# Performance work log

Measured on AMD Instinct MI355X. Metric: run time of the kernel, lower is better.

## Reference

```python
import jax, jax.numpy as jnp
import numpy as np

FRAME = 1024
HOP = 512
BATCH = 64
SAMPLES = 1 << 20


def _make_windows():
    # periodic Hann window; COLA with hop=FRAME//2, normalization constant = 1.0
    n = jnp.arange(FRAME, dtype=jnp.float32)
    w = 0.5 * (1.0 - jnp.cos(2.0 * jnp.pi * n / FRAME))
    # edge_correction loop: only h_idx=1 is non-empty for hop = frame/2
    pre = w.at[: FRAME - HOP].add(w[HOP:])
    post = w.at[HOP:].add(w[: FRAME - HOP])
    # normalize_window with normalization = 1.0 is a no-op; mode='wola' -> sqrt
    return jnp.sqrt(w), jnp.sqrt(pre), jnp.sqrt(post)


def setup_inputs() -> dict:
    key = jax.random.key(0)
    x = jax.random.normal(key, (BATCH, SAMPLES), dtype=jnp.float32)
    w, pre, post = _make_windows()
    return {
        "x": x,
        "window": w,
        "prewindow": pre,
        "postwindow": post,
        "hop_size": HOP,
        "frame_size": FRAME,
    }


def reference(x, window, prewindow, postwindow, hop_size, frame_size):
    # number_of_segments = samples//hop - frame//hop + 1 (as in _segment)
    n_samples = x.shape[1]
    n_seg = n_samples // hop_size - frame_size // hop_size + 1
    # strided gather: idx[k, j] = k*hop + j  -> frames [B, S, F]
    idx = jnp.arange(n_seg)[:, None] * hop_size + jnp.arange(frame_size)[None, :]
    frames = x[:, idx]
    # per-segment window matrix: row 0 = prewindow, last = postwindow, middle = window
    W = jnp.concatenate(
        [
            prewindow[None, :],
            jnp.broadcast_to(window, (n_seg - 2, frame_size)),
            postwindow[None, :],
        ],
        axis=0,
    )
    return frames * W[None, :, :]
```

## Files before the change

kernel.cpp:

```cpp
#include <hip/hip_runtime.h>

constexpr int FRAME   = 1024;
constexpr int HOP     = 512;
constexpr int BATCH   = 64;
constexpr int SAMPLES = 1 << 20;
constexpr int NSEG    = SAMPLES / HOP - FRAME / HOP + 1;
constexpr int F4      = FRAME / 4;
constexpr int H4      = HOP / 4;
constexpr int S4      = SAMPLES / 4;

__global__ __launch_bounds__(256) void seg_win_kernel(
    const float4* __restrict__ x,
    const float4* __restrict__ win,
    const float4* __restrict__ pre,
    const float4* __restrict__ post,
    float4* __restrict__ out)
{
    const int blk = blockIdx.x;
    const int s   = blk % NSEG;
    const int b   = blk / NSEG;

    const float4* __restrict__ w =
        (s == 0) ? pre : (s == NSEG - 1) ? post : win;

    const int f = threadIdx.x;

    const float4 wv = w[f];
    const float4 xv = x[(size_t)b * S4 + (size_t)s * H4 + f];

    float4 o;
    o.x = xv.x * wv.x;
    o.y = xv.y * wv.y;
    o.z = xv.z * wv.z;
    o.w = xv.w * wv.w;

    out[(size_t)blk * F4 + f] = o;
}

extern "C" void kernel_launch(void* const* d_in, const int* in_sizes, int n_in,
                              void* d_out, int out_size, void* d_ws, size_t ws_size,
                              hipStream_t stream)
{
    const float4* x    = (const float4*)d_in[0];
    const float4* win  = (const float4*)d_in[1];
    const float4* pre  = (const float4*)d_in[2];
    const float4* post = (const float4*)d_in[3];
    float4* out        = (float4*)d_out;

    dim3 grid(BATCH * NSEG);
    dim3 block(F4);
    seg_win_kernel<<<grid, block, 0, stream>>>(x, win, pre, post, out);
}
```

Baseline: 691.4 us.

## Read each input hop once and scatter to both overlapping frames with nontemporal access

```diff
diff --git a/kernel.cpp b/kernel.cpp
--- a/kernel.cpp
+++ b/kernel.cpp
@@ -9,45 +9,55 @@
 constexpr int H4      = HOP / 4;
 constexpr int S4      = SAMPLES / 4;
 
-__global__ __launch_bounds__(256) void seg_win_kernel(
-    const float4* __restrict__ x,
-    const float4* __restrict__ win,
-    const float4* __restrict__ pre,
-    const float4* __restrict__ post,
-    float4* __restrict__ out)
+typedef float f32x4 __attribute__((ext_vector_type(4)));
+
+__global__ __launch_bounds__(256) void seg_win_hop_kernel(
+    const f32x4* __restrict__ x,
+    const f32x4* __restrict__ win,
+    const f32x4* __restrict__ pre,
+    const f32x4* __restrict__ post,
+    f32x4* __restrict__ out)
 {
-    const int blk = blockIdx.x;
-    const int s   = blk % NSEG;
-    const int b   = blk / NSEG;
+    const size_t gid = (size_t)blockIdx.x * 256 + threadIdx.x;
+    const int b  = (int)(gid >> 18);
+    const int j4 = (int)(gid & (S4 - 1));
+    const int h  = j4 >> 7;
+    const int r  = j4 & (H4 - 1);
 
-    const float4* __restrict__ w =
-        (s == 0) ? pre : (s == NSEG - 1) ? post : win;
+    const f32x4 xv = __builtin_nontemporal_load(&x[gid]);
 
-    const int f = threadIdx.x;
+    const size_t out_row_base = (size_t)b * NSEG;
 
-    const float4 wv = w[f];
-    const float4 xv = x[(size_t)b * S4 + (size_t)s * H4 + f];
+    if (h <= NSEG - 1) {
+        const int s = h;
+        const f32x4* __restrict__ w =
+            (s == 0) ? pre : (s == NSEG - 1) ? post : win;
+        const f32x4 wv = w[r];
+        const f32x4 o = xv * wv;
+        __builtin_nontemporal_store(o, &out[(out_row_base + s) * F4 + r]);
+    }
 
-    float4 o;
-    o.x = xv.x * wv.x;
-    o.y = xv.y * wv.y;
-    o.z = xv.z * wv.z;
-    o.w = xv.w * wv.w;
-
-    out[(size_t)blk * F4 + f] = o;
+    if (h >= 1) {
+        const int s = h - 1;
+        const f32x4* __restrict__ w =
+            (s == 0) ? pre : (s == NSEG - 1) ? post : win;
+        const f32x4 wv = w[r + H4];
+        const f32x4 o = xv * wv;
+        __builtin_nontemporal_store(o, &out[(out_row_base + s) * F4 + r + H4]);
+    }
 }
 
 extern "C" void kernel_launch(void* const* d_in, const int* in_sizes, int n_in,
                               void* d_out, int out_size, void* d_ws, size_t ws_size,
                               hipStream_t stream)
 {
-    const float4* x    = (const float4*)d_in[0];
-    const float4* win  = (const float4*)d_in[1];
-    const float4* pre  = (const float4*)d_in[2];
-    const float4* post = (const float4*)d_in[3];
-    float4* out        = (float4*)d_out;
+    const f32x4* x    = (const f32x4*)d_in[0];
+    const f32x4* win  = (const f32x4*)d_in[1];
+    const f32x4* pre  = (const f32x4*)d_in[2];
+    const f32x4* post = (const f32x4*)d_in[3];
+    f32x4* out        = (f32x4*)d_out;
 
-    dim3 grid(BATCH * NSEG);
-    dim3 block(F4);
-    seg_win_kernel<<<grid, block, 0, stream>>>(x, win, pre, post, out);
+    dim3 grid((BATCH * (size_t)S4) / 256);
+    dim3 block(256);
+    seg_win_hop_kernel<<<grid, block, 0, stream>>>(x, win, pre, post, out);
 }
```

Measured after the change: 671.2 us. 1.03x faster.
